# Kernel optimization log

Hardware: AMD Instinct MI355X
Metric: run time of the kernel (lower is better)

The kernel has to match this reference:

```python
import jax, jax.numpy as jnp
import numpy as np

SIGMA = 0.2


def setup_inputs() -> dict:
    key = jax.random.key(0)
    ks = jax.random.split(key, 16)
    N = 200000
    corner = jax.random.normal(ks[0], (N, 9), dtype=jnp.float32)
    normal = jax.random.normal(ks[1], (N, 3), dtype=jnp.float32)
    neighbour = jax.random.randint(ks[2], (N, 3), 0, N, dtype=jnp.int32)
    # Face_Rotate_Conv params: Conv1d(1,32,6,stride=3), Linear(32,64), Linear(64,64)
    conv_w = jax.random.normal(ks[3], (32, 1, 6), dtype=jnp.float32) * 0.3
    conv_b = jax.random.normal(ks[4], (32,), dtype=jnp.float32) * 0.1
    l3_w = jax.random.normal(ks[5], (64, 32), dtype=jnp.float32) * 0.15
    l3_b = jax.random.normal(ks[6], (64,), dtype=jnp.float32) * 0.05
    l4_w = jax.random.normal(ks[7], (64, 64), dtype=jnp.float32) * 0.12
    l4_b = jax.random.normal(ks[8], (64,), dtype=jnp.float32) * 0.05
    # Kernel_Correlation params: theta ~ U(0,pi), phi ~ U(0,2pi), shape [1,64,4]
    theta = jax.random.uniform(ks[9], (1, 64, 4), dtype=jnp.float32) * np.float32(np.pi)
    phi = jax.random.uniform(ks[10], (1, 64, 4), dtype=jnp.float32) * np.float32(2 * np.pi)
    # trailing 1x1 conv / bn / 1x1 conv on 131 channels
    c1_w = jax.random.normal(ks[11], (131, 131, 1), dtype=jnp.float32) * 0.08
    c1_b = jax.random.normal(ks[12], (131,), dtype=jnp.float32) * 0.05
    c2_w = jax.random.normal(ks[13], (131, 131, 1), dtype=jnp.float32) * 0.08
    c2_b = jax.random.normal(ks[14], (131,), dtype=jnp.float32) * 0.05
    bn_g = jnp.ones((131,), dtype=jnp.float32)
    bn_b = jnp.zeros((131,), dtype=jnp.float32)
    return {"corner": corner, "normal": normal, "neighbour": neighbour,
            "conv_w": conv_w, "conv_b": conv_b, "l3_w": l3_w, "l3_b": l3_b,
            "l4_w": l4_w, "l4_b": l4_b, "theta": theta, "phi": phi,
            "c1_w": c1_w, "c1_b": c1_b, "c2_w": c2_w, "c2_b": c2_b,
            "bn_g": bn_g, "bn_b": bn_b}


def reference(corner, normal, neighbour, conv_w, conv_b, l3_w, l3_b, l4_w, l4_b,
              theta, phi, c1_w, c1_b, c2_w, c2_b, bn_g, bn_b):
    # ---- Face_Rotate_Conv ----
    # cat(c1,c2,c3,c1) -> [n,12]; conv1d k=6 stride=3 over length 12 -> 3 windows
    arr = jnp.concatenate([corner[:, 0:3], corner[:, 3:6], corner[:, 6:9], corner[:, 0:3]], axis=1)
    patches = jnp.stack([arr[:, 0:6], arr[:, 3:9], arr[:, 6:12]], axis=1)  # [n,3,6]
    conv_out = jnp.einsum('npk,ok->npo', patches, conv_w[:, 0, :]) + conv_b  # [n,3,32]
    frc = conv_out.mean(axis=1)  # [n,32] (mean over output length == mean over windows)
    h = jax.nn.relu(frc @ l3_w.T + l3_b)
    x = h @ l4_w.T + l4_b  # [n,64]
    # ---- Kernel_Correlation ----
    nb = neighbour.astype(jnp.int32)
    f = jnp.stack([normal, normal[nb[:, 0]], normal[nb[:, 1]], normal[nb[:, 2]]], axis=2)  # [n,3,4]
    th, ph = theta[0], phi[0]  # [64,4]
    kern = jnp.stack([jnp.sin(th) * jnp.sin(ph), jnp.sin(th) * jnp.cos(ph), jnp.cos(th)], axis=0)  # [3,64,4]
    # ||f - k||^2 over xyz expanded via |f|^2 + |k|^2 - 2 f.k (avoids [n,3,64,4,4])
    f2 = jnp.sum(f * f, axis=1)   # [n,4]
    k2 = jnp.sum(kern * kern, axis=0)  # [64,4]
    cross = jnp.einsum('nca,cmb->nmab', f, kern)  # [n,64,4,4]
    correl = f2[:, None, :, None] + k2[None, :, None, :] - 2.0 * cross
    z = jnp.exp(correl / (-2.0 * SIGMA * SIGMA)).sum(axis=(2, 3)) / 16.0  # [n,64]
    # ---- structural_Des head ----
    feat = jnp.concatenate([normal, x, z], axis=1)  # [n,131]
    y = feat @ c1_w[:, :, 0].T + c1_b  # 1x1 conv == linear
    mu = y.mean(axis=0)
    var = y.var(axis=0)  # biased var, matches train-mode BatchNorm1d
    y = jax.nn.relu((y - mu) / jnp.sqrt(var + 1e-5) * bn_g + bn_b)
    out = y @ c2_w[:, :, 0].T + c2_b
    return out  # [n,131]
```

## Files before the change

### kernel.cpp

```cpp
#include <hip/hip_runtime.h>
#include <math.h>

typedef __attribute__((ext_vector_type(8))) short short8;
typedef _Float16 half8 __attribute__((ext_vector_type(8)));
typedef __attribute__((ext_vector_type(4))) float f32x4;
typedef __attribute__((ext_vector_type(2))) uint uint2v;
typedef unsigned int uint;
typedef unsigned short ushort;

#define N_PTS 200000
#define N_PAD 200064
#define NBLK  1563
#define YST   168
#define ZK    (-18.033688011112043f)
#define C2K   (36.067376022224086f)


#define FEAT_OFF  0ull
#define WT1_OFF   118437888ull
#define WT2_OFF   118483968ull
#define KERN2_OFF 118530048ull
#define WSUM_OFF  118534144ull
#define L3H_OFF   118534528ull
#define L4H_OFF   118538624ull
#define GSUM_OFF  118546816ull
#define GSQ_OFF   118547456ull

__device__ inline ushort f2h(float x) {
    return __builtin_bit_cast(ushort, (_Float16)x);
}
__device__ inline uint pack2h(float a, float b) {
    return __builtin_bit_cast(uint, __builtin_amdgcn_cvt_pkrtz(a, b));
}

__global__ void sdes_k0_setup(const float* __restrict__ conv_w, const float* __restrict__ l3w,
                              const float* __restrict__ l4w, const float* __restrict__ theta,
                              const float* __restrict__ phi, const float* __restrict__ c1w,
                              const float* __restrict__ c2w,
                              float* wsumT, ushort* l3h, ushort* l4h, float* kern2,
                              ushort* WT1t, ushort* WT2t, float* gsum, float* gsq)
{
    const int t = threadIdx.x, b = blockIdx.x;
    if (b == 90) {
        for (int i = t; i < 96; i += 256) {
            int k = i >> 5, o = i & 31;
            wsumT[k * 32 + o] = conv_w[o * 6 + k] + conv_w[o * 6 + k + 3];
        }
        for (int i = t; i < 2048; i += 256) l3h[i] = f2h(l3w[i]);
        for (int i = t; i < 4096; i += 256) l4h[i] = f2h(l4w[i]);
        int m = t >> 2, bb = t & 3;
        float th = theta[m * 4 + bb], ph = phi[m * 4 + bb];
        float st = sinf(th), ct = cosf(th), sp = sinf(ph), cp = cosf(ph);
        kern2[m * 16 + bb * 4 + 0] = st * sp * C2K;
        kern2[m * 16 + bb * 4 + 1] = st * cp * C2K;
        kern2[m * 16 + bb * 4 + 2] = ct * C2K;
        kern2[m * 16 + bb * 4 + 3] = 0.f;
        return;
    }
    if (b == 0 && t < 160) { gsum[t] = 0.f; gsq[t] = 0.f; }
    int i = b * 256 + t;
    if (i >= 144 * 160) return;
    int e = i & 7, l = (i >> 3) & 63, rem = i >> 9;
    int kc = rem % 5, tc = rem / 5;
    int n = tc * 16 + (l & 15);
    int k = kc * 32 + (l >> 4) * 8 + e;
    float v = 0.f;
    if (n < 131) {
        if (k < 64)       v = c1w[n * 131 + 3 + k];
        else if (k < 128) v = c1w[n * 131 + 67 + (k - 64)];
        else if (k < 131) v = c1w[n * 131 + (k - 128)];
    }
    WT1t[i] = f2h(v);
    float v2 = (n < 131 && k < 131) ? c2w[n * 131 + k] : 0.f;
    WT2t[i] = f2h(v2);
}

#define FST 40
#define W3T 40
#define W4T 72
__global__ __launch_bounds__(640) void sdes_k1ab(
    const float* __restrict__ corner, const float* __restrict__ conv_b,
    const float* __restrict__ wsumT, const ushort* __restrict__ l3h,
    const float* __restrict__ l3b, const ushort* __restrict__ l4h,
    const float* __restrict__ l4b,
    const float* __restrict__ normal, const int* __restrict__ neigh,
    const float* __restrict__ kern2g, ushort* __restrict__ feat)
{
    __shared__ __align__(16) ushort frcS[128 * FST];
    __shared__ __align__(16) ushort hS[128 * 64];
    __shared__ __align__(16) ushort w3S[64 * W3T];
    __shared__ __align__(16) ushort w4S[64 * W4T];
    __shared__ __align__(16) float fS[128 * 17];
    __shared__ float wsL[96], cbL[32], b3L[64], b4L[64];
    const int t = threadIdx.x;

    if (t < 128) {
        int p0g = blockIdx.x * 128 + t;
        int pg = p0g < N_PTS ? p0g : N_PTS - 1;
        float g0[4], g1[4], g2[4];
        g0[0] = normal[(size_t)pg * 3 + 0]; g1[0] = normal[(size_t)pg * 3 + 1]; g2[0] = normal[(size_t)pg * 3 + 2];
        int nb0 = neigh[(size_t)pg * 3 + 0];
        int nb1 = neigh[(size_t)pg * 3 + 1];
        int nb2 = neigh[(size_t)pg * 3 + 2];
        g0[1] = normal[(size_t)nb0 * 3 + 0]; g1[1] = normal[(size_t)nb0 * 3 + 1]; g2[1] = normal[(size_t)nb0 * 3 + 2];
        g0[2] = normal[(size_t)nb1 * 3 + 0]; g1[2] = normal[(size_t)nb1 * 3 + 1]; g2[2] = normal[(size_t)nb1 * 3 + 2];
        g0[3] = normal[(size_t)nb2 * 3 + 0]; g1[3] = normal[(size_t)nb2 * 3 + 1]; g2[3] = normal[(size_t)nb2 * 3 + 2];
        float* fp = &fS[t * 17];
        #pragma unroll
        for (int a = 0; a < 4; ++a) {
            fp[a]      = g0[a];
            fp[4 + a]  = g1[a];
            fp[8 + a]  = g2[a];
            fp[12 + a] = (g0[a]*g0[a] + g1[a]*g1[a] + g2[a]*g2[a] + 1.0f) * ZK;
        }
    }

    for (int i = t; i < 96; i += 640) wsL[i] = wsumT[i];
    for (int i = t; i < 32; i += 640) cbL[i] = conv_b[i];
    for (int i = t; i < 64; i += 640) { b3L[i] = l3b[i]; b4L[i] = l4b[i]; }
    for (int i = t; i < 256; i += 640) {
        int c = i >> 2, kc = i & 3;
        *(uint4*)&w3S[c * W3T + kc * 8] = *(const uint4*)&l3h[c * 32 + kc * 8];
    }
    for (int i = t; i < 512; i += 640) {
        int c = i >> 3, kc = i & 7;
        *(uint4*)&w4S[c * W4T + kc * 8] = *(const uint4*)&l4h[c * 64 + kc * 8];
    }
    __syncthreads();

    if (t < 512) {
        const int g  = t >> 7;
        const int tt = g & 1;
        const int uu = g >> 1;
        const int pi = t & 127;
        const int p0 = blockIdx.x * 128 + pi;
        const int rt = p0 >> 4, pl = p0 & 15;
        const float* fp = &fS[pi * 17];
        float f0[4], f1[4], f2v[4], base[4];
        #pragma unroll
        for (int a = 0; a < 4; ++a) {
            f0[a] = fp[a]; f1[a] = fp[4 + a]; f2v[a] = fp[8 + a]; base[a] = fp[12 + a];
        }
        const size_t tbase = ((size_t)(rt * 5 + 2 + tt)) * 512;
        #pragma unroll
        for (int qi = 0; qi < 2; ++qi) {
            const int qq = uu * 2 + qi;
            float zv[8];
            #pragma unroll
            for (int mm = 0; mm < 8; ++mm) {
                int m = (tt * 4 + qq) * 8 + mm;
                const float* kp = kern2g + m * 16;
                float a0 = 0.f, a1 = 0.f, a2 = 0.f, a3 = 0.f;
                #pragma unroll
                for (int b = 0; b < 4; ++b) {
                    float kx = kp[b * 4 + 0], ky = kp[b * 4 + 1], kz = kp[b * 4 + 2];
                    a0 += __builtin_amdgcn_exp2f(fmaf(f0[0], kx, fmaf(f1[0], ky, fmaf(f2v[0], kz, base[0]))));
                    a1 += __builtin_amdgcn_exp2f(fmaf(f0[1], kx, fmaf(f1[1], ky, fmaf(f2v[1], kz, base[1]))));
                    a2 += __builtin_amdgcn_exp2f(fmaf(f0[2], kx, fmaf(f1[2], ky, fmaf(f2v[2], kz, base[2]))));
                    a3 += __builtin_amdgcn_exp2f(fmaf(f0[3], kx, fmaf(f1[3], ky, fmaf(f2v[3], kz, base[3]))));
                }
                zv[mm] = ((a0 + a1) + (a2 + a3)) * (1.f / 16.f);
            }
            uint4 v;
            v.x = pack2h(zv[0], zv[1]); v.y = pack2h(zv[2], zv[3]);
            v.z = pack2h(zv[4], zv[5]); v.w = pack2h(zv[6], zv[7]);
            *(uint4*)(feat + tbase + (pl + 16 * qq) * 8) = v;
        }
        {
            size_t base4 = ((size_t)(rt * 5 + 4)) * 512;
            if (g == 0) {
                uint4 v;
                v.x = pack2h(f0[0], f1[0]); v.y = pack2h(f2v[0], 0.f); v.z = 0u; v.w = 0u;
                *(uint4*)(feat + base4 + pl * 8) = v;
            } else {
                const uint4 zz = {0u, 0u, 0u, 0u};
                *(uint4*)(feat + base4 + (pl + 16 * g) * 8) = zz;
            }
        }
        return;
    }

    const int tm = t - 512;
    {
        int row = blockIdx.x * 128 + tm;
        int p = row < N_PTS ? row : N_PTS - 1;
        const float* cp = corner + (size_t)p * 9;
        float c0 = cp[0], c1 = cp[1], c2 = cp[2], c3 = cp[3], c4 = cp[4],
              c5 = cp[5], c6 = cp[6], c7 = cp[7], c8 = cp[8];
        float mp0 = (c0 + c3 + c6) * (1.f / 3.f);
        float mp1 = (c1 + c4 + c7) * (1.f / 3.f);
        float mp2 = (c2 + c5 + c8) * (1.f / 3.f);
        #pragma unroll
        for (int o = 0; o < 32; o += 2) {
            float g0 = fmaf(mp0, wsL[o], fmaf(mp1, wsL[32 + o], fmaf(mp2, wsL[64 + o], cbL[o])));
            float g1 = fmaf(mp0, wsL[o+1], fmaf(mp1, wsL[33 + o], fmaf(mp2, wsL[65 + o], cbL[o+1])));
            *(uint*)&frcS[tm * FST + o] = pack2h(g0, g1);
        }
    }

    const int lane = tm & 63, w = tm >> 6;
    const int rbase = w * 64;
    const int rlo = lane & 15, kg = lane >> 4;
    const f32x4 z4 = {0.f, 0.f, 0.f, 0.f};

    {
        half8 af[4], bf[4];
        #pragma unroll
        for (int rt = 0; rt < 4; ++rt)
            af[rt] = *(const half8*)&frcS[(rbase + rt * 16 + rlo) * FST + kg * 8];
        #pragma unroll
        for (int tc = 0; tc < 4; ++tc)
            bf[tc] = *(const half8*)&w3S[(tc * 16 + rlo) * W3T + kg * 8];
        #pragma unroll
        for (int rt = 0; rt < 4; ++rt) {
            #pragma unroll
            for (int tc = 0; tc < 4; ++tc) {
                f32x4 acc = __builtin_amdgcn_mfma_f32_16x16x32_f16(af[rt], bf[tc], z4, 0, 0, 0);
                int col = tc * 16 + rlo;
                float bias = b3L[col];
                #pragma unroll
                for (int r = 0; r < 4; ++r) {
                    int hrow = rbase + rt * 16 + kg * 4 + r;
                    float v = fmaxf(acc[r] + bias, 0.f);
                    int sc = (((col >> 3) ^ (hrow & 7)) << 3) | (col & 7);
                    hS[hrow * 64 + sc] = f2h(v);
                }
            }
        }
    }

    {
        f32x4 acc4[4][4];
        #pragma unroll
        for (int pt = 0; pt < 4; ++pt)
            #pragma unroll
            for (int tc = 0; tc < 4; ++tc) acc4[pt][tc] = z4;
        #pragma unroll
        for (int ks = 0; ks < 2; ++ks) {
            half8 af[4], bf[4];
            #pragma unroll
            for (int pt = 0; pt < 4; ++pt) {
                int row = rbase + pt * 16 + rlo;
                int blk = (ks * 4 + kg) ^ (rlo & 7);
                af[pt] = *(const half8*)&hS[row * 64 + blk * 8];
            }
            #pragma unroll
            for (int tc = 0; tc < 4; ++tc)
                bf[tc] = *(const half8*)&w4S[(tc * 16 + rlo) * W4T + ks * 32 + kg * 8];
            #pragma unroll
            for (int pt = 0; pt < 4; ++pt)
                #pragma unroll
                for (int tc = 0; tc < 4; ++tc)
                    acc4[pt][tc] = __builtin_amdgcn_mfma_f32_16x16x32_f16(bf[tc], af[pt], acc4[pt][tc], 0, 0, 0);
        }
        #pragma unroll
        for (int pt = 0; pt < 4; ++pt) {
            int rtg = blockIdx.x * 8 + w * 4 + pt;
            #pragma unroll
            for (int tc = 0; tc < 4; ++tc) {
                int xb = tc * 16 + kg * 4;
                float v0 = acc4[pt][tc][0] + b4L[xb + 0];
                float v1 = acc4[pt][tc][1] + b4L[xb + 1];
                float v2 = acc4[pt][tc][2] + b4L[xb + 2];
                float v3 = acc4[pt][tc][3] + b4L[xb + 3];
                uint2v st; st.x = pack2h(v0, v1); st.y = pack2h(v2, v3);
                int kc = tc >> 1;
                int l = rlo + 16 * ((2 * tc + (kg >> 1)) & 3);
                size_t off = ((size_t)(rtg * 5 + kc)) * 512 + l * 8 + (kg & 1) * 4;
                *(uint2v*)(feat + off) = st;
            }
        }
    }
}

__global__ __launch_bounds__(1024, 4) void sdes_k2_stats(
    const ushort* __restrict__ FT, const ushort* __restrict__ WT1t,
    const float* __restrict__ c1b, float* __restrict__ gsum, float* __restrict__ gsq)
{
    __shared__ __align__(16) ushort W1s[45 * 512];
    __shared__ float sS[144], sQ[144];
    const int t = threadIdx.x;
    const int lane = t & 63, wv = t >> 6;
    const int b = blockIdx.x;
    const int s = b * 16 + wv;
    const int rlo = lane & 15, kg = lane >> 4;

    const int cnt = 3 + ((wv == 0 && b < 216) ? 1 : 0);
    const int start = 3 * s + (b < 216 ? b : 216) + ((b < 216 && wv > 0) ? 1 : 0);

    half8 afA[5], afB[5];
    #pragma unroll
    for (int kc = 0; kc < 5; ++kc)
        afA[kc] = *(const half8*)(FT + ((size_t)start * 5 + kc) * 512 + lane * 8);

    for (int i = t; i < 2880; i += 1024) ((uint4*)W1s)[i] = ((const uint4*)WT1t)[i];
    if (t < 144) { sS[t] = 0.f; sQ[t] = 0.f; }
    __syncthreads();

    float sreg[9], qreg[9], bL[9];
    #pragma unroll
    for (int tc = 0; tc < 9; ++tc) {
        sreg[tc] = 0.f; qreg[tc] = 0.f;
        int n = tc * 16 + rlo;
        bL[tc] = (n < 131) ? c1b[n] : 0.f;
    }

    for (int it = 0; it < cnt; ++it) {
        const int p = start + it;
        f32x4 acc[9];
        #pragma unroll
        for (int tc = 0; tc < 9; ++tc) acc[tc] = (f32x4){0.f, 0.f, 0.f, 0.f};
        #pragma unroll
        for (int kc = 0; kc < 5; ++kc) {
            #pragma unroll
            for (int tc = 0; tc < 9; ++tc) {
                half8 bw = *(const half8*)(W1s + (tc * 5 + kc) * 512 + lane * 8);
                acc[tc] = __builtin_amdgcn_mfma_f32_16x16x32_f16(afA[kc], bw, acc[tc], 0, 0, 0);
            }
        }
        if (it + 1 < cnt) {
            #pragma unroll
            for (int kc = 0; kc < 5; ++kc)
                afB[kc] = *(const half8*)(FT + ((size_t)(p + 1) * 5 + kc) * 512 + lane * 8);
            __builtin_amdgcn_sched_barrier(0);
        }
        const int row0 = p * 16;
        #pragma unroll
        for (int tc = 0; tc < 9; ++tc) {
            float b0 = bL[tc];
            #pragma unroll
            for (int r = 0; r < 4; ++r) {
                int grow = row0 + kg * 4 + r;
                if (grow < N_PTS) {
                    float v = acc[tc][r] + b0;
                    sreg[tc] += v;
                    qreg[tc] = fmaf(v, v, qreg[tc]);
                }
            }
        }
        #pragma unroll
        for (int kc = 0; kc < 5; ++kc) afA[kc] = afB[kc];
    }

    #pragma unroll
    for (int tc = 0; tc < 9; ++tc) {
        float sv = sreg[tc], qv = qreg[tc];
        sv += __shfl_xor(sv, 16);  sv += __shfl_xor(sv, 32);
        qv += __shfl_xor(qv, 16);  qv += __shfl_xor(qv, 32);
        if (lane < 16) {
            int n = tc * 16 + rlo;
            atomicAdd(&sS[n], sv); atomicAdd(&sQ[n], qv);
        }
    }
    __syncthreads();
    if (t < 144) { atomicAdd(&gsum[t], sS[t]); atomicAdd(&gsq[t], sQ[t]); }
}

__global__ __launch_bounds__(768, 3) void sdes_k3_fused(
    const ushort* __restrict__ FT, const ushort* __restrict__ WT1t,
    const ushort* __restrict__ WT2t, const float* __restrict__ c1b,
    const float* __restrict__ gsum, const float* __restrict__ gsq,
    const float* __restrict__ bng, const float* __restrict__ bnb,
    const float* __restrict__ c2b, float* __restrict__ out)
{
    __shared__ __align__(16) ushort Ws[2 * 45 * 512];
    __shared__ __align__(16) ushort yS[192 * YST];
    __shared__ __align__(16) float scL[160], shL[160], b1L[160], c2L[160];
    const int t = threadIdx.x;
    const int lane = t & 63, wv = t >> 6;
    const int rlo = lane & 15, kg = lane >> 4;
    const int b = blockIdx.x;
    const int s = b * 12 + wv;

    const int cnt = 2 + ((wv == 0 && b < 108) ? 1 : 0);
    const int start = 2 * s + (b < 108 ? b : 108) + ((b < 108 && wv > 0) ? 1 : 0);

    half8 afA[5][2], afB[5][2];
    #pragma unroll
    for (int kc = 0; kc < 5; ++kc)
        #pragma unroll
        for (int pt = 0; pt < 2; ++pt)
            afA[kc][pt] = *(const half8*)(FT + ((size_t)(start * 2 + pt) * 5 + kc) * 512 + lane * 8);

    for (int i = t; i < 5760; i += 768) ((uint4*)Ws)[i] = ((const uint4*)WT1t)[i];

    if (t < 160) {
        float sc = 0.f, sh = 0.f, bb = 0.f, c2 = 0.f;
        if (t < 131) {
            float mu = gsum[t] * (1.f / 200000.f);
            float var = gsq[t] * (1.f / 200000.f) - mu * mu;
            sc = bng[t] / sqrtf(var + 1e-5f);
            sh = bnb[t] - mu * sc;
            bb = c1b[t]; c2 = c2b[t];
        }
        scL[t] = sc; shL[t] = sh; b1L[t] = bb; c2L[t] = c2;
    }
    __syncthreads();

    const half8 hz = {0, 0, 0, 0, 0, 0, 0, 0};
    ushort* slab = yS + wv * 16 * YST;

    for (int it = 0; it < cnt; ++it) {
        const int p = start + it;

        f32x4 acc[2][9];
        #pragma unroll
        for (int pt = 0; pt < 2; ++pt)
            #pragma unroll
            for (int tc = 0; tc < 9; ++tc) acc[pt][tc] = (f32x4){0.f, 0.f, 0.f, 0.f};
        #pragma unroll
        for (int kc = 0; kc < 5; ++kc) {
            #pragma unroll
            for (int tc = 0; tc < 9; ++tc) {
                half8 bw = *(const half8*)(Ws + (tc * 5 + kc) * 512 + lane * 8);
                #pragma unroll
                for (int pt = 0; pt < 2; ++pt)
                    acc[pt][tc] = __builtin_amdgcn_mfma_f32_16x16x32_f16(afA[kc][pt], bw, acc[pt][tc], 0, 0, 0);
            }
        }

        if (it + 1 < cnt) {
            #pragma unroll
            for (int kc = 0; kc < 5; ++kc)
                #pragma unroll
                for (int pt = 0; pt < 2; ++pt)
                    afB[kc][pt] = *(const half8*)(FT + ((size_t)((p + 1) * 2 + pt) * 5 + kc) * 512 + lane * 8);
            __builtin_amdgcn_sched_barrier(0);
        }

        const int row0 = p * 32;
        #pragma unroll
        for (int pt = 0; pt < 2; ++pt) {
            #pragma unroll
            for (int tc = 0; tc < 9; ++tc) {
                int n = tc * 16 + rlo;
                float sc = scL[n], sh = shL[n], bb = b1L[n];
                #pragma unroll
                for (int r = 0; r < 4; ++r) {
                    float v = fmaxf(fmaf(acc[pt][tc][r] + bb, sc, sh), 0.f);
                    slab[(kg * 4 + r) * YST + n] = f2h(v);
                }
            }

            f32x4 acc2[9];
            #pragma unroll
            for (int tc = 0; tc < 9; ++tc) acc2[tc] = (f32x4){0.f, 0.f, 0.f, 0.f};
            #pragma unroll
            for (int kc2 = 0; kc2 < 5; ++kc2) {
                bool vld = (kc2 < 4) || (kg < 2);
                half8 af2 = vld ? *(const half8*)&slab[rlo * YST + kc2 * 32 + kg * 8] : hz;
                #pragma unroll
                for (int tc = 0; tc < 9; ++tc) {
                    half8 bw = *(const half8*)(Ws + 23040 + (tc * 5 + kc2) * 512 + lane * 8);
                    acc2[tc] = __builtin_amdgcn_mfma_f32_16x16x32_f16(bw, af2, acc2[tc], 0, 0, 0);
                }
            }
            const int prow = row0 + pt * 16 + rlo;
            if (prow < N_PTS) {
                float* op = out + (size_t)prow * 131;
                #pragma unroll
                for (int tc = 0; tc < 8; ++tc) {
                    const int c0 = tc * 16 + kg * 4;
                    f32x4 vv = acc2[tc] + *(const f32x4*)&c2L[c0];
                    __builtin_memcpy(op + c0, &vv, 16);
                }
                if (kg == 0) {
                    op[128] = acc2[8][0] + c2L[128];
                    op[129] = acc2[8][1] + c2L[129];
                    op[130] = acc2[8][2] + c2L[130];
                }
            }
        }

        #pragma unroll
        for (int kc = 0; kc < 5; ++kc)
            #pragma unroll
            for (int pt = 0; pt < 2; ++pt)
                afA[kc][pt] = afB[kc][pt];
    }
}

extern "C" void kernel_launch(void* const* d_in, const int* in_sizes, int n_in,
                              void* d_out, int out_size, void* d_ws, size_t ws_size,
                              hipStream_t stream) {
    const float* corner = (const float*)d_in[0];
    const float* normal = (const float*)d_in[1];
    const int*   neigh  = (const int*)d_in[2];
    const float* conv_w = (const float*)d_in[3];
    const float* conv_b = (const float*)d_in[4];
    const float* l3_w   = (const float*)d_in[5];
    const float* l3_b   = (const float*)d_in[6];
    const float* l4_w   = (const float*)d_in[7];
    const float* l4_b   = (const float*)d_in[8];
    const float* theta  = (const float*)d_in[9];
    const float* phi    = (const float*)d_in[10];
    const float* c1_w   = (const float*)d_in[11];
    const float* c1_b   = (const float*)d_in[12];
    const float* c2_w   = (const float*)d_in[13];
    const float* c2_b   = (const float*)d_in[14];
    const float* bn_g   = (const float*)d_in[15];
    const float* bn_b   = (const float*)d_in[16];

    char* ws = (char*)d_ws;
    ushort* feat  = (ushort*)(ws + FEAT_OFF);
    ushort* WT1t  = (ushort*)(ws + WT1_OFF);
    ushort* WT2t  = (ushort*)(ws + WT2_OFF);
    float*  kern2 = (float*)(ws + KERN2_OFF);
    float*  wsumT = (float*)(ws + WSUM_OFF);
    ushort* l3h   = (ushort*)(ws + L3H_OFF);
    ushort* l4h   = (ushort*)(ws + L4H_OFF);
    float*  gsum  = (float*)(ws + GSUM_OFF);
    float*  gsq   = (float*)(ws + GSQ_OFF);

    sdes_k0_setup<<<91, 256, 0, stream>>>(conv_w, l3_w, l4_w, theta, phi, c1_w, c2_w,
                                          wsumT, l3h, l4h, kern2, WT1t, WT2t, gsum, gsq);
    sdes_k1ab<<<NBLK, 640, 0, stream>>>(corner, conv_b, wsumT, l3h, l3_b, l4h, l4_b,
                                        normal, neigh, kern2, feat);
    sdes_k2_stats<<<256, 1024, 0, stream>>>(feat, WT1t, c1_b, gsum, gsq);
    sdes_k3_fused<<<256, 768, 0, stream>>>(feat, WT1t, WT2t, c1_b, gsum, gsq,
                                           bn_g, bn_b, c2_b, (float*)d_out);
}
```

Baseline: 132.4 us.

## Fuse BatchNorm statistics pass into feature-building kernel, dropping separate stats kernel

Folds the first 1x1 conv and the per-channel sum and sum-of-squares accumulation into the feature kernel k1ab. After a block barrier, the 128 MLP threads reread the just-written feat tiles, which should still be in cache, and run the MFMA against WT1t straight from global memory. That removes a full extra pass over the feature buffer and one kernel launch. In exchange, WT1t is no longer staged in shared memory, only 128 threads per block do the stats GEMM, and global atomics grow from 256 blocks to 1563 blocks with no block-level reduction first.

Result: slower. 297.1 us (+124.4%).

```diff
diff --git a/kernel.cpp b/kernel.cpp
--- a/kernel.cpp
+++ b/kernel.cpp
@@ -78,13 +78,15 @@
 #define FST 40
 #define W3T 40
 #define W4T 72
-__global__ __launch_bounds__(640) void sdes_k1ab(
+__global__ __launch_bounds__(640, 5) void sdes_k1ab(
     const float* __restrict__ corner, const float* __restrict__ conv_b,
     const float* __restrict__ wsumT, const ushort* __restrict__ l3h,
     const float* __restrict__ l3b, const ushort* __restrict__ l4h,
     const float* __restrict__ l4b,
     const float* __restrict__ normal, const int* __restrict__ neigh,
-    const float* __restrict__ kern2g, ushort* __restrict__ feat)
+    const float* __restrict__ kern2g, ushort* __restrict__ feat,
+    const ushort* __restrict__ WT1t, const float* __restrict__ c1b,
+    float* __restrict__ gsum, float* __restrict__ gsq)
 {
     __shared__ __align__(16) ushort frcS[128 * FST];
     __shared__ __align__(16) ushort hS[128 * 64];
@@ -177,183 +179,162 @@
                 *(uint4*)(feat + base4 + (pl + 16 * g) * 8) = zz;
             }
         }
-        return;
-    }
-
-    const int tm = t - 512;
-    {
-        int row = blockIdx.x * 128 + tm;
-        int p = row < N_PTS ? row : N_PTS - 1;
-        const float* cp = corner + (size_t)p * 9;
-        float c0 = cp[0], c1 = cp[1], c2 = cp[2], c3 = cp[3], c4 = cp[4],
-              c5 = cp[5], c6 = cp[6], c7 = cp[7], c8 = cp[8];
-        float mp0 = (c0 + c3 + c6) * (1.f / 3.f);
-        float mp1 = (c1 + c4 + c7) * (1.f / 3.f);
-        float mp2 = (c2 + c5 + c8) * (1.f / 3.f);
-        #pragma unroll
-        for (int o = 0; o < 32; o += 2) {
-            float g0 = fmaf(mp0, wsL[o], fmaf(mp1, wsL[32 + o], fmaf(mp2, wsL[64 + o], cbL[o])));
-            float g1 = fmaf(mp0, wsL[o+1], fmaf(mp1, wsL[33 + o], fmaf(mp2, wsL[65 + o], cbL[o+1])));
-            *(uint*)&frcS[tm * FST + o] = pack2h(g0, g1);
-        }
-    }
-
-    const int lane = tm & 63, w = tm >> 6;
-    const int rbase = w * 64;
-    const int rlo = lane & 15, kg = lane >> 4;
-    const f32x4 z4 = {0.f, 0.f, 0.f, 0.f};
-
-    {
-        half8 af[4], bf[4];
-        #pragma unroll
-        for (int rt = 0; rt < 4; ++rt)
-            af[rt] = *(const half8*)&frcS[(rbase + rt * 16 + rlo) * FST + kg * 8];
-        #pragma unroll
-        for (int tc = 0; tc < 4; ++tc)
-            bf[tc] = *(const half8*)&w3S[(tc * 16 + rlo) * W3T + kg * 8];
-        #pragma unroll
-        for (int rt = 0; rt < 4; ++rt) {
-            #pragma unroll
-            for (int tc = 0; tc < 4; ++tc) {
-                f32x4 acc = __builtin_amdgcn_mfma_f32_16x16x32_f16(af[rt], bf[tc], z4, 0, 0, 0);
-                int col = tc * 16 + rlo;
-                float bias = b3L[col];
-                #pragma unroll
-                for (int r = 0; r < 4; ++r) {
-                    int hrow = rbase + rt * 16 + kg * 4 + r;
-                    float v = fmaxf(acc[r] + bias, 0.f);
-                    int sc = (((col >> 3) ^ (hrow & 7)) << 3) | (col & 7);
-                    hS[hrow * 64 + sc] = f2h(v);
-                }
-            }
-        }
-    }
-
-    {
-        f32x4 acc4[4][4];
-        #pragma unroll
-        for (int pt = 0; pt < 4; ++pt)
-            #pragma unroll
-            for (int tc = 0; tc < 4; ++tc) acc4[pt][tc] = z4;
-        #pragma unroll
-        for (int ks = 0; ks < 2; ++ks) {
+    } else {
+        const int tm = t - 512;
+        {
+            int row = blockIdx.x * 128 + tm;
+            int p = row < N_PTS ? row : N_PTS - 1;
+            const float* cp = corner + (size_t)p * 9;
+            float c0 = cp[0], c1 = cp[1], c2 = cp[2], c3 = cp[3], c4 = cp[4],
+                  c5 = cp[5], c6 = cp[6], c7 = cp[7], c8 = cp[8];
+            float mp0 = (c0 + c3 + c6) * (1.f / 3.f);
+            float mp1 = (c1 + c4 + c7) * (1.f / 3.f);
+            float mp2 = (c2 + c5 + c8) * (1.f / 3.f);
+            #pragma unroll
+            for (int o = 0; o < 32; o += 2) {
+                float g0 = fmaf(mp0, wsL[o], fmaf(mp1, wsL[32 + o], fmaf(mp2, wsL[64 + o], cbL[o])));
+                float g1 = fmaf(mp0, wsL[o+1], fmaf(mp1, wsL[33 + o], fmaf(mp2, wsL[65 + o], cbL[o+1])));
+                *(uint*)&frcS[tm * FST + o] = pack2h(g0, g1);
+            }
+        }
+
+        const int lane = tm & 63, w = tm >> 6;
+        const int rbase = w * 64;
+        const int rlo = lane & 15, kg = lane >> 4;
+        const f32x4 z4 = {0.f, 0.f, 0.f, 0.f};
+
+        {
             half8 af[4], bf[4];
             #pragma unroll
+            for (int rt = 0; rt < 4; ++rt)
+                af[rt] = *(const half8*)&frcS[(rbase + rt * 16 + rlo) * FST + kg * 8];
+            #pragma unroll
+            for (int tc = 0; tc < 4; ++tc)
+                bf[tc] = *(const half8*)&w3S[(tc * 16 + rlo) * W3T + kg * 8];
+            #pragma unroll
+            for (int rt = 0; rt < 4; ++rt) {
+                #pragma unroll
+                for (int tc = 0; tc < 4; ++tc) {
+                    f32x4 acc = __builtin_amdgcn_mfma_f32_16x16x32_f16(af[rt], bf[tc], z4, 0, 0, 0);
+                    int col = tc * 16 + rlo;
+                    float bias = b3L[col];
+                    #pragma unroll
+                    for (int r = 0; r < 4; ++r) {
+                        int hrow = rbase + rt * 16 + kg * 4 + r;
+                        float v = fmaxf(acc[r] + bias, 0.f);
+                        int sc = (((col >> 3) ^ (hrow & 7)) << 3) | (col & 7);
+                        hS[hrow * 64 + sc] = f2h(v);
+                    }
+                }
+            }
+        }
+
+        {
+            f32x4 acc4[4][4];
+            #pragma unroll
+            for (int pt = 0; pt < 4; ++pt)
+                #pragma unroll
+                for (int tc = 0; tc < 4; ++tc) acc4[pt][tc] = z4;
+            #pragma unroll
+            for (int ks = 0; ks < 2; ++ks) {
+                half8 af[4], bf[4];
+                #pragma unroll
+                for (int pt = 0; pt < 4; ++pt) {
+                    int row = rbase + pt * 16 + rlo;
+                    int blk = (ks * 4 + kg) ^ (rlo & 7);
+                    af[pt] = *(const half8*)&hS[row * 64 + blk * 8];
+                }
+                #pragma unroll
+                for (int tc = 0; tc < 4; ++tc)
+                    bf[tc] = *(const half8*)&w4S[(tc * 16 + rlo) * W4T + ks * 32 + kg * 8];
+                #pragma unroll
+                for (int pt = 0; pt < 4; ++pt)
+                    #pragma unroll
+                    for (int tc = 0; tc < 4; ++tc)
+                        acc4[pt][tc] = __builtin_amdgcn_mfma_f32_16x16x32_f16(bf[tc], af[pt], acc4[pt][tc], 0, 0, 0);
+            }
+            #pragma unroll
             for (int pt = 0; pt < 4; ++pt) {
-                int row = rbase + pt * 16 + rlo;
-                int blk = (ks * 4 + kg) ^ (rlo & 7);
-                af[pt] = *(const half8*)&hS[row * 64 + blk * 8];
-            }
-            #pragma unroll
-            for (int tc = 0; tc < 4; ++tc)
-                bf[tc] = *(const half8*)&w4S[(tc * 16 + rlo) * W4T + ks * 32 + kg * 8];
-            #pragma unroll
-            for (int pt = 0; pt < 4; ++pt)
-                #pragma unroll
-                for (int tc = 0; tc < 4; ++tc)
-                    acc4[pt][tc] = __builtin_amdgcn_mfma_f32_16x16x32_f16(bf[tc], af[pt], acc4[pt][tc], 0, 0, 0);
-        }
-        #pragma unroll
-        for (int pt = 0; pt < 4; ++pt) {
-            int rtg = blockIdx.x * 8 + w * 4 + pt;
-            #pragma unroll
-            for (int tc = 0; tc < 4; ++tc) {
-                int xb = tc * 16 + kg * 4;
-                float v0 = acc4[pt][tc][0] + b4L[xb + 0];
-                float v1 = acc4[pt][tc][1] + b4L[xb + 1];
-                float v2 = acc4[pt][tc][2] + b4L[xb + 2];
-                float v3 = acc4[pt][tc][3] + b4L[xb + 3];
-                uint2v st; st.x = pack2h(v0, v1); st.y = pack2h(v2, v3);
-                int kc = tc >> 1;
-                int l = rlo + 16 * ((2 * tc + (kg >> 1)) & 3);
-                size_t off = ((size_t)(rtg * 5 + kc)) * 512 + l * 8 + (kg & 1) * 4;
-                *(uint2v*)(feat + off) = st;
-            }
-        }
-    }
-}
-
-__global__ __launch_bounds__(1024, 4) void sdes_k2_stats(
-    const ushort* __restrict__ FT, const ushort* __restrict__ WT1t,
-    const float* __restrict__ c1b, float* __restrict__ gsum, float* __restrict__ gsq)
-{
-    __shared__ __align__(16) ushort W1s[45 * 512];
-    __shared__ float sS[144], sQ[144];
-    const int t = threadIdx.x;
-    const int lane = t & 63, wv = t >> 6;
-    const int b = blockIdx.x;
-    const int s = b * 16 + wv;
-    const int rlo = lane & 15, kg = lane >> 4;
-
-    const int cnt = 3 + ((wv == 0 && b < 216) ? 1 : 0);
-    const int start = 3 * s + (b < 216 ? b : 216) + ((b < 216 && wv > 0) ? 1 : 0);
-
-    half8 afA[5], afB[5];
-    #pragma unroll
-    for (int kc = 0; kc < 5; ++kc)
-        afA[kc] = *(const half8*)(FT + ((size_t)start * 5 + kc) * 512 + lane * 8);
-
-    for (int i = t; i < 2880; i += 1024) ((uint4*)W1s)[i] = ((const uint4*)WT1t)[i];
-    if (t < 144) { sS[t] = 0.f; sQ[t] = 0.f; }
+                int rtg = blockIdx.x * 8 + w * 4 + pt;
+                #pragma unroll
+                for (int tc = 0; tc < 4; ++tc) {
+                    int xb = tc * 16 + kg * 4;
+                    float v0 = acc4[pt][tc][0] + b4L[xb + 0];
+                    float v1 = acc4[pt][tc][1] + b4L[xb + 1];
+                    float v2 = acc4[pt][tc][2] + b4L[xb + 2];
+                    float v3 = acc4[pt][tc][3] + b4L[xb + 3];
+                    uint2v st; st.x = pack2h(v0, v1); st.y = pack2h(v2, v3);
+                    int kc = tc >> 1;
+                    int l = rlo + 16 * ((2 * tc + (kg >> 1)) & 3);
+                    size_t off = ((size_t)(rtg * 5 + kc)) * 512 + l * 8 + (kg & 1) * 4;
+                    *(uint2v*)(feat + off) = st;
+                }
+            }
+        }
+    }
+
     __syncthreads();
 
-    float sreg[9], qreg[9], bL[9];
-    #pragma unroll
-    for (int tc = 0; tc < 9; ++tc) {
-        sreg[tc] = 0.f; qreg[tc] = 0.f;
-        int n = tc * 16 + rlo;
-        bL[tc] = (n < 131) ? c1b[n] : 0.f;
-    }
-
-    for (int it = 0; it < cnt; ++it) {
-        const int p = start + it;
-        f32x4 acc[9];
-        #pragma unroll
-        for (int tc = 0; tc < 9; ++tc) acc[tc] = (f32x4){0.f, 0.f, 0.f, 0.f};
-        #pragma unroll
-        for (int kc = 0; kc < 5; ++kc) {
-            #pragma unroll
-            for (int tc = 0; tc < 9; ++tc) {
-                half8 bw = *(const half8*)(W1s + (tc * 5 + kc) * 512 + lane * 8);
-                acc[tc] = __builtin_amdgcn_mfma_f32_16x16x32_f16(afA[kc], bw, acc[tc], 0, 0, 0);
-            }
-        }
-        if (it + 1 < cnt) {
+    if (t >= 512) {
+        const int tm2 = t - 512;
+        const int lane = tm2 & 63, w = tm2 >> 6;
+        const int rlo = lane & 15, kg = lane >> 4;
+        float sreg[9], qreg[9];
+        #pragma unroll
+        for (int tc = 0; tc < 9; ++tc) { sreg[tc] = 0.f; qreg[tc] = 0.f; }
+        #pragma unroll
+        for (int i = 0; i < 4; ++i) {
+            const int rt = blockIdx.x * 8 + w * 4 + i;
+            const int row0 = rt * 16;
+            half8 af[5];
             #pragma unroll
             for (int kc = 0; kc < 5; ++kc)
-                afB[kc] = *(const half8*)(FT + ((size_t)(p + 1) * 5 + kc) * 512 + lane * 8);
-            __builtin_amdgcn_sched_barrier(0);
-        }
-        const int row0 = p * 16;
+                af[kc] = *(const half8*)(feat + ((size_t)rt * 5 + kc) * 512 + lane * 8);
+            #pragma unroll
+            for (int h = 0; h < 2; ++h) {
+                f32x4 acc[5];
+                #pragma unroll
+                for (int j = 0; j < 5; ++j) acc[j] = (f32x4){0.f, 0.f, 0.f, 0.f};
+                #pragma unroll
+                for (int kc = 0; kc < 5; ++kc) {
+                    #pragma unroll
+                    for (int j = 0; j < 5; ++j) {
+                        if (h == 1 && j == 4) continue;
+                        const int tc = h * 5 + j;
+                        half8 bw = *(const half8*)(WT1t + ((size_t)tc * 5 + kc) * 512 + lane * 8);
+                        acc[j] = __builtin_amdgcn_mfma_f32_16x16x32_f16(af[kc], bw, acc[j], 0, 0, 0);
+                    }
+                }
+                #pragma unroll
+                for (int j = 0; j < 5; ++j) {
+                    if (h == 1 && j == 4) continue;
+                    const int tc = h * 5 + j;
+                    const int n = tc * 16 + rlo;
+                    float b0 = (n < 131) ? c1b[n] : 0.f;
+                    #pragma unroll
+                    for (int r = 0; r < 4; ++r) {
+                        int grow = row0 + kg * 4 + r;
+                        if (grow < N_PTS) {
+                            float v = acc[j][r] + b0;
+                            sreg[tc] += v;
+                            qreg[tc] = fmaf(v, v, qreg[tc]);
+                        }
+                    }
+                }
+            }
+        }
         #pragma unroll
         for (int tc = 0; tc < 9; ++tc) {
-            float b0 = bL[tc];
-            #pragma unroll
-            for (int r = 0; r < 4; ++r) {
-                int grow = row0 + kg * 4 + r;
-                if (grow < N_PTS) {
-                    float v = acc[tc][r] + b0;
-                    sreg[tc] += v;
-                    qreg[tc] = fmaf(v, v, qreg[tc]);
-                }
-            }
-        }
-        #pragma unroll
-        for (int kc = 0; kc < 5; ++kc) afA[kc] = afB[kc];
-    }
-
-    #pragma unroll
-    for (int tc = 0; tc < 9; ++tc) {
-        float sv = sreg[tc], qv = qreg[tc];
-        sv += __shfl_xor(sv, 16);  sv += __shfl_xor(sv, 32);
-        qv += __shfl_xor(qv, 16);  qv += __shfl_xor(qv, 32);
-        if (lane < 16) {
-            int n = tc * 16 + rlo;
-            atomicAdd(&sS[n], sv); atomicAdd(&sQ[n], qv);
-        }
-    }
-    __syncthreads();
-    if (t < 144) { atomicAdd(&gsum[t], sS[t]); atomicAdd(&gsq[t], sQ[t]); }
+            float sv = sreg[tc], qv = qreg[tc];
+            sv += __shfl_xor(sv, 16);  sv += __shfl_xor(sv, 32);
+            qv += __shfl_xor(qv, 16);  qv += __shfl_xor(qv, 32);
+            if (lane < 16) {
+                int n = tc * 16 + rlo;
+                atomicAdd(&gsum[n], sv);
+                atomicAdd(&gsq[n], qv);
+            }
+        }
+    }
 }
 
 __global__ __launch_bounds__(768, 3) void sdes_k3_fused(
@@ -515,8 +496,7 @@
     sdes_k0_setup<<<91, 256, 0, stream>>>(conv_w, l3_w, l4_w, theta, phi, c1_w, c2_w,
                                           wsumT, l3h, l4h, kern2, WT1t, WT2t, gsum, gsq);
     sdes_k1ab<<<NBLK, 640, 0, stream>>>(corner, conv_b, wsumT, l3h, l3_b, l4h, l4_b,
-                                        normal, neigh, kern2, feat);
-    sdes_k2_stats<<<256, 1024, 0, stream>>>(feat, WT1t, c1_b, gsum, gsq);
+                                        normal, neigh, kern2, feat, WT1t, c1_b, gsum, gsq);
     sdes_k3_fused<<<256, 768, 0, stream>>>(feat, WT1t, WT2t, c1_b, gsum, gsq,
                                            bn_g, bn_b, c2_b, (float*)d_out);
 }
```
